# Optimization experiments

Measured on AMD Instinct MI355X. Metric: run time of the kernel, lower is better.

The kernel has to match this reference:

```python
import jax, jax.numpy as jnp
import numpy as np

B_SZ, L_SEQ, D_MODEL, D_STATE = 4, 2048, 1024, 16


def setup_inputs() -> dict:
    key = jax.random.key(0)
    ks = jax.random.split(key, 6)
    x = jax.random.normal(ks[0], (B_SZ, L_SEQ, D_MODEL), jnp.float32)
    # HiPPO-inspired init: A_log = log(arange(1..n)).clamp(min=-7), broadcast over channels
    A_log = jnp.clip(jnp.log(jnp.arange(1, D_STATE + 1, dtype=jnp.float32)), -7.0, None)
    A_log = jnp.broadcast_to(A_log[None, :], (D_MODEL, D_STATE)).astype(jnp.float32)
    B_param = 0.02 * jax.random.normal(ks[1], (D_MODEL, D_STATE), jnp.float32)
    C_param = 0.02 * jax.random.normal(ks[2], (D_MODEL, D_STATE), jnp.float32)
    log_dt = 0.01 * jax.random.normal(ks[3], (D_MODEL,), jnp.float32) - 4.0
    in_w = jax.random.normal(ks[4], (2 * D_MODEL, D_MODEL), jnp.float32) / np.sqrt(D_MODEL).astype(np.float32)
    in_b = jnp.zeros((2 * D_MODEL,), jnp.float32)
    out_w = jax.random.normal(ks[5], (D_MODEL, D_MODEL), jnp.float32) / np.sqrt(D_MODEL).astype(np.float32)
    out_b = jnp.zeros((D_MODEL,), jnp.float32)
    ln_g = jnp.ones((D_MODEL,), jnp.float32)
    ln_b = jnp.zeros((D_MODEL,), jnp.float32)
    return {"x": x, "A_log": A_log, "B_param": B_param, "C_param": C_param,
            "log_dt": log_dt, "in_w": in_w, "in_b": in_b, "out_w": out_w,
            "out_b": out_b, "ln_g": ln_g, "ln_b": ln_b}


def _ssm_scan(u, A_log, B_param, C_param, log_dt):
    # u: (B, L, D). Builds kernel h[t,d] = sum_n A_bar[d,n]^t * C[d,n]*B[d,n]*dt[d]
    # and applies a causal depthwise convolution (via FFT; same math as conv1d).
    L = u.shape[1]
    dt = jnp.clip(jnp.exp(log_dt), 1e-4, 1.0)                      # (D,)
    A_bar = jnp.exp(-jnp.exp(A_log) * dt[:, None])                 # ZOH discretisation (D,N)
    A_bar = jnp.clip(A_bar, 1e-8, 1.0 - 1e-8)
    log_A = jnp.log(A_bar)                                         # (D,N)
    t_idx = jnp.arange(L, dtype=jnp.float32)                       # (L,)
    A_powers = jnp.exp(t_idx[:, None, None] * log_A[None, :, :])   # (L,D,N)
    cb_dt = C_param * B_param * dt[:, None]                        # (D,N)
    kernel = jnp.einsum('ldn,dn->ld', A_powers, cb_dt)             # (L,D)
    # causal conv: y[b,t,d] = sum_{tau<=t} kernel[tau,d] * u[b,t-tau,d]
    n_fft = 2 * L
    Kf = jnp.fft.rfft(kernel, n=n_fft, axis=0)                     # (n_fft/2+1, D)
    Uf = jnp.fft.rfft(u, n=n_fft, axis=1)                          # (B, n_fft/2+1, D)
    y = jnp.fft.irfft(Uf * Kf[None], n=n_fft, axis=1)[:, :L]       # (B,L,D)
    return y.astype(u.dtype)


def reference(x, A_log, B_param, C_param, log_dt, in_w, in_b, out_w, out_b, ln_g, ln_b):
    x = x.astype(jnp.float32)
    residual = x
    # LayerNorm (eps=1e-5)
    mu = jnp.mean(x, axis=-1, keepdims=True)
    var = jnp.mean(jnp.square(x - mu), axis=-1, keepdims=True)
    xn = (x - mu) * jax.lax.rsqrt(var + 1e-5) * ln_g + ln_b
    xz = xn @ in_w.T + in_b                                        # (B,L,2D)
    x_proj, z = xz[..., :D_MODEL], xz[..., D_MODEL:]
    z = jax.nn.silu(z)
    y = _ssm_scan(x_proj, A_log, B_param, C_param, log_dt)
    y = y * z
    y = y @ out_w.T + out_b
    # dropout is identity in eval mode
    return jnp.clip(y + residual, -10.0, 10.0)
```

## Files before the change

### kernel.cpp

```cpp
#include <hip/hip_runtime.h>
#include <hip/hip_bf16.h>

#define D_MODEL 1024
#define D_STATE 16
#define L_SEQ 2048
#define B_SZ 4
#define M_ROWS (B_SZ * L_SEQ)
#define N_CHUNK 32
#define C_LEN 64

typedef __attribute__((ext_vector_type(8))) short short8;
typedef __attribute__((ext_vector_type(4))) float f32x4;

#define SBAR()  asm volatile("s_barrier" ::: "memory")
#define GATE(N) asm volatile("s_waitcnt vmcnt(" #N ") lgkmcnt(0)\n\ts_barrier" ::: "memory")

typedef const unsigned short __attribute__((address_space(1))) gas_us;
typedef unsigned short __attribute__((address_space(3))) las_us;
static __device__ __forceinline__ void gload16(const unsigned short* g, unsigned short* l) {
    __builtin_amdgcn_global_load_lds((gas_us*)g, (las_us*)l, 16, 0, 0);
}

static __device__ __forceinline__ unsigned short f2bf(float f) {
    unsigned int u = __float_as_uint(f);
    unsigned int r = (u + 0x7FFFu + ((u >> 16) & 1u)) >> 16;
    return (unsigned short)r;
}
static __device__ __forceinline__ float bf2f(unsigned short u) {
    return __uint_as_float(((unsigned int)u) << 16);
}

__global__ __launch_bounds__(256) void prep_kernel(const float* __restrict__ x,
                                                   const float* __restrict__ g,
                                                   const float* __restrict__ b,
                                                   unsigned short* __restrict__ xn,
                                                   const float* __restrict__ in_w,
                                                   unsigned short* __restrict__ w1,
                                                   const float* __restrict__ out_w,
                                                   unsigned short* __restrict__ w2) {
    __shared__ float sbuf[8];
    int bid = blockIdx.x;
    int t = threadIdx.x;
    if (bid < M_ROWS) {
        int row = bid;
        const float4* xr = (const float4*)(x + (size_t)row * D_MODEL);
        float4 v = xr[t];
        float s  = v.x + v.y + v.z + v.w;
        float ss = v.x * v.x + v.y * v.y + v.z * v.z + v.w * v.w;
        #pragma unroll
        for (int o = 32; o > 0; o >>= 1) {
            s  += __shfl_down(s,  o);
            ss += __shfl_down(ss, o);
        }
        int wid = t >> 6;
        if ((t & 63) == 0) { sbuf[wid] = s; sbuf[4 + wid] = ss; }
        __syncthreads();
        float S  = sbuf[0] + sbuf[1] + sbuf[2] + sbuf[3];
        float SS = sbuf[4] + sbuf[5] + sbuf[6] + sbuf[7];
        float mu  = S * (1.0f / D_MODEL);
        float var = SS * (1.0f / D_MODEL) - mu * mu;
        float inv = rsqrtf(var + 1e-5f);
        float4 gv = ((const float4*)g)[t];
        float4 bv = ((const float4*)b)[t];
        ushort4 o;
        o.x = f2bf((v.x - mu) * inv * gv.x + bv.x);
        o.y = f2bf((v.y - mu) * inv * gv.y + bv.y);
        o.z = f2bf((v.z - mu) * inv * gv.z + bv.z);
        o.w = f2bf((v.w - mu) * inv * gv.w + bv.w);
        ((ushort4*)(xn + (size_t)row * D_MODEL))[t] = o;
    } else if (bid < M_ROWS + 2048) {
        int i = (bid - M_ROWS) * 256 + t;
        float4 v = ((const float4*)in_w)[i];
        ushort4 o;
        o.x = f2bf(v.x); o.y = f2bf(v.y); o.z = f2bf(v.z); o.w = f2bf(v.w);
        ((ushort4*)w1)[i] = o;
    } else {
        int i = (bid - M_ROWS - 2048) * 256 + t;
        float4 v = ((const float4*)out_w)[i];
        ushort4 o;
        o.x = f2bf(v.x); o.y = f2bf(v.y); o.z = f2bf(v.z); o.w = f2bf(v.w);
        ((ushort4*)w2)[i] = o;
    }
}

#define STG(B_, MAT_, KH_, GPTR_, KOFF_) do { \
    unsigned short* d_ = lbase + (B_)*32768 + (MAT_)*16384 + (KH_)*8192 + wave*1024; \
    gload16((GPTR_) + (KOFF_), d_); \
    gload16((GPTR_) + 16*K + (KOFF_), d_ + 512); } while(0)

#define PH(B_, KS_, MG_, READB_, STAGE_, TAIL_) { \
    if (READB_) { \
        _Pragma("unroll") for (int j_ = 0; j_ < 4; ++j_) \
            bv[j_] = *(const short8*)(ldsB + (B_)*65536 + (KS_)*16384 + (wn*4 + j_)*1024); \
    } \
    short8 av[4]; \
    _Pragma("unroll") for (int i_ = 0; i_ < 4; ++i_) \
        av[i_] = *(const short8*)(ldsA + (B_)*65536 + (KS_)*16384 + (wm*8 + (MG_)*4 + i_)*1024); \
    STAGE_; \
    SBAR(); \
    asm volatile("s_waitcnt lgkmcnt(0)" ::: "memory"); \
    __builtin_amdgcn_s_setprio(1); \
    _Pragma("unroll") for (int i_ = 0; i_ < 4; ++i_) { \
        _Pragma("unroll") for (int j_ = 0; j_ < 4; ++j_) \
            acc[(MG_)*4 + i_][j_] = __builtin_amdgcn_mfma_f32_16x16x32_bf16( \
                av[i_], bv[j_], acc[(MG_)*4 + i_][j_], 0, 0, 0); } \
    __builtin_amdgcn_s_setprio(0); \
    TAIL_; \
}

__global__ __launch_bounds__(512, 1) void gemm1_kernel(const unsigned short* __restrict__ A,
                                                       const unsigned short* __restrict__ Bt,
                                                       const float* __restrict__ bias,
                                                       unsigned short* __restrict__ u_bf,
                                                       unsigned short* __restrict__ zs) {
    __shared__ __align__(16) unsigned short lds[2][32768];
    const int K = D_MODEL;

    int t = threadIdx.x;
    int lane = t & 63;
    int wave = t >> 6;
    int wm = wave >> 2;
    int wn = wave & 3;

    int bid = blockIdx.x;
    int swz = (bid & 7) * 32 + (bid >> 3);
    int m0 = (swz >> 3) * 256;
    int n0 = (swz & 7) * 256;

    int srow = lane >> 2;
    int sk = ((lane & 3) * 8) ^ ((lane & 32) >> 1);
    const unsigned short* gA = A  + (size_t)(m0 + wave * 32 + srow) * K + sk;
    const unsigned short* gB = Bt + (size_t)(n0 + wave * 32 + srow) * K + sk;

    unsigned short* lbase = &lds[0][0];

    int off_base = (lane & 15) * 64 + (((lane >> 4) * 16) ^ ((lane & 8) * 4));
    const char* ldsA = (const char*)lbase + off_base;
    const char* ldsB = (const char*)lbase + 32768 + off_base;

    f32x4 acc[8][4] = {};
    short8 bv[4];

    STG(0, 0, 0, gA, 0);  STG(0, 1, 0, gB, 0);
    STG(0, 0, 1, gA, 32); STG(0, 1, 1, gB, 32);
    STG(1, 0, 0, gA, 64); STG(1, 1, 0, gB, 64);
    GATE(4);

    int ko = 0;
    #pragma unroll 1
    for (int it = 0; it < 7; ++it) {
        PH(0, 0, 0, true,  STG(1, 0, 1, gA, ko + 96),  SBAR());
        PH(0, 0, 1, false, STG(1, 1, 1, gB, ko + 96),  SBAR());
        PH(0, 1, 0, true,  STG(0, 0, 0, gA, ko + 128), SBAR());
        PH(0, 1, 1, false, STG(0, 1, 0, gB, ko + 128), GATE(4));
        PH(1, 0, 0, true,  STG(0, 0, 1, gA, ko + 160), SBAR());
        PH(1, 0, 1, false, STG(0, 1, 1, gB, ko + 160), SBAR());
        PH(1, 1, 0, true,  STG(1, 0, 0, gA, ko + 192), SBAR());
        PH(1, 1, 1, false, STG(1, 1, 0, gB, ko + 192), GATE(4));
        ko += 128;
    }
    PH(0, 0, 0, true,  STG(1, 0, 1, gA, ko + 96), SBAR());
    PH(0, 0, 1, false, STG(1, 1, 1, gB, ko + 96), SBAR());
    PH(0, 1, 0, true,  (void)0, SBAR());
    PH(0, 1, 1, false, (void)0, GATE(0));
    PH(1, 0, 0, true,  (void)0, SBAR());
    PH(1, 0, 1, false, (void)0, SBAR());
    PH(1, 1, 0, true,  (void)0, SBAR());
    PH(1, 1, 1, false, (void)0, (void)0);

    int col = lane & 15;
    int quad = lane >> 4;
    float bs[4];
    #pragma unroll
    for (int jf = 0; jf < 4; ++jf) bs[jf] = bias[n0 + wn * 64 + jf * 16 + col];
    bool isU = (n0 < D_MODEL);
    int nbase = isU ? (n0 + wn * 64 + col) : (n0 - D_MODEL + wn * 64 + col);
    unsigned short* obase = isU ? u_bf : zs;
    #pragma unroll
    for (int i = 0; i < 8; ++i) {
        #pragma unroll
        for (int r = 0; r < 4; ++r) {
            int m = m0 + wm * 128 + i * 16 + quad * 4 + r;
            unsigned short* orow = obase + (size_t)m * D_MODEL + nbase;
            #pragma unroll
            for (int jf = 0; jf < 4; ++jf) {
                float v = acc[i][jf][r] + bs[jf];
                if (!isU) v = v / (1.0f + __expf(-v));
                orow[jf * 16] = f2bf(v);
            }
        }
    }
}

#define MFMA16(ACC, AV, BV) { \
    _Pragma("unroll") for (int i_ = 0; i_ < 4; ++i_) { \
        _Pragma("unroll") for (int jf_ = 0; jf_ < 4; ++jf_) \
            ACC[i_][jf_] = __builtin_amdgcn_mfma_f32_16x16x32_bf16( \
                AV[i_], BV[jf_], ACC[i_][jf_], 0, 0, 0); } }

#define STAGE2(J) { size_t ko_ = (size_t)(J) * 32; int so_ = ((J) & 3) * 12288; \
    gload16(pA0 + ko_, dA + so_); gload16(pB0 + ko_, dB0 + so_); gload16(pB1 + ko_, dB1 + so_); }

#define G2_TILE(J, DOSTAGE, TRAIL) { \
    const int slot_ = (J) & 3; \
    const char* rA_ = ldsA_rd + slot_ * 24576; \
    const char* rB_ = ldsB_rd + slot_ * 24576; \
    short8 av[4], bv[4]; \
    _Pragma("unroll") for (int i_ = 0; i_ < 4; ++i_) av[i_] = *(const short8*)(rA_ + i_ * 1024); \
    _Pragma("unroll") for (int j_ = 0; j_ < 4; ++j_) bv[j_] = *(const short8*)(rB_ + j_ * 1024); \
    if (DOSTAGE) { STAGE2((J) + 3); } \
    SBAR(); \
    __builtin_amdgcn_s_setprio(1); \
    MFMA16(acc, av, bv); \
    __builtin_amdgcn_s_setprio(0); \
    TRAIL; \
}

__global__ __launch_bounds__(512, 2) void gemm2_kernel(const unsigned short* __restrict__ A,
                                                       const unsigned short* __restrict__ Bt,
                                                       const float* __restrict__ bias,
                                                       float* __restrict__ out_f,
                                                       const float* __restrict__ resid) {
    __shared__ __align__(16) unsigned short lds[4][12288];
    const int K = D_MODEL;

    int t = threadIdx.x;
    int lane = t & 63;
    int wave = t >> 6;
    int wm = wave >> 2;
    int wn = wave & 3;

    int bid = blockIdx.x;
    int swz = (bid & 7) * 32 + (bid >> 3);
    int m0 = (swz >> 2) * 128;
    int n0 = (swz & 3) * 256;

    int srow = lane >> 2;
    int sk = ((lane & 3) * 8) ^ ((lane & 32) >> 1);
    const unsigned short* pA0 = A  + (size_t)(m0 + wave * 16 + srow) * K + sk;
    const unsigned short* pB0 = Bt + (size_t)(n0 + wave * 16 + srow) * K + sk;
    const unsigned short* pB1 = pB0 + (size_t)128 * K;

    unsigned short* dA  = &lds[0][wave * 512];
    unsigned short* dB0 = &lds[0][4096 + wave * 512];
    unsigned short* dB1 = &lds[0][8192 + wave * 512];

    int off_base = (lane & 15) * 64 + (((lane >> 4) * 16) ^ ((lane & 8) * 4));
    const char* ldsA_rd = (const char*)(&lds[0][0]) + wm * 4096 + off_base;
    const char* ldsB_rd = (const char*)(&lds[0][0]) + 8192 + wn * 4096 + off_base;

    f32x4 acc[4][4] = {};

    STAGE2(0); STAGE2(1); STAGE2(2);
    GATE(6);

    #pragma unroll 1
    for (int j = 0; j < 29; ++j) { G2_TILE(j, true, GATE(6)); }
    G2_TILE(29, false, GATE(3));
    G2_TILE(30, false, GATE(0));
    G2_TILE(31, false, (void)0);

    int col = lane & 15;
    int quad = lane >> 4;
    float bs[4];
    #pragma unroll
    for (int jf = 0; jf < 4; ++jf) bs[jf] = bias[n0 + wn * 64 + jf * 16 + col];
    #pragma unroll
    for (int i = 0; i < 4; ++i) {
        #pragma unroll
        for (int r = 0; r < 4; ++r) {
            int m = m0 + wm * 64 + i * 16 + quad * 4 + r;
            const float* rrow = resid + (size_t)m * D_MODEL + n0 + wn * 64 + col;
            float* orow = out_f + (size_t)m * D_MODEL + n0 + wn * 64 + col;
            #pragma unroll
            for (int jf = 0; jf < 4; ++jf) {
                float y = acc[i][jf][r] + bs[jf] + rrow[jf * 16];
                y = fminf(10.0f, fmaxf(-10.0f, y));
                orow[jf * 16] = y;
            }
        }
    }
}

__global__ __launch_bounds__(512) void scan_fused_kernel(const unsigned short* __restrict__ u,
                                                         const unsigned short* __restrict__ zs,
                                                         const float* __restrict__ A_log,
                                                         const float* __restrict__ Bp,
                                                         const float* __restrict__ Cp,
                                                         const float* __restrict__ log_dt,
                                                         unsigned short* __restrict__ yz) {
    __shared__ float S[N_CHUNK][D_STATE][17];

    int bid = blockIdx.x;
    int l  = (bid & 7) * 32 + (bid >> 3);
    int b  = l >> 6;
    int dg = l & 63;
    int t  = threadIdx.x;
    int c  = t >> 4;
    int dl = t & 15;
    int d  = dg * 16 + dl;

    float dt = fminf(1.0f, fmaxf(1e-4f, __expf(log_dt[d])));
    float ab[D_STATE];
    #pragma unroll
    for (int n = 0; n < D_STATE; n++) {
        float a = __expf(-__expf(A_log[d * D_STATE + n]) * dt);
        ab[n] = fminf(1.0f - 1e-8f, fmaxf(1e-8f, a));
    }

    size_t row0 = (size_t)(b * L_SEQ + c * C_LEN);
    const unsigned short* up = u + row0 * D_MODEL + d;

    unsigned int uc[32];
    float P[D_STATE];
    #pragma unroll
    for (int n = 0; n < D_STATE; n++) P[n] = 0.0f;
    #pragma unroll
    for (int tt = 0; tt < 32; tt++) {
        unsigned int lo = up[(size_t)(2 * tt) * D_MODEL];
        unsigned int hi = up[(size_t)(2 * tt + 1) * D_MODEL];
        uc[tt] = lo | (hi << 16);
        float u0 = __uint_as_float(lo << 16);
        float u1 = __uint_as_float(hi << 16);
        #pragma unroll
        for (int n = 0; n < D_STATE; n++) P[n] = fmaf(ab[n], P[n], u0);
        #pragma unroll
        for (int n = 0; n < D_STATE; n++) P[n] = fmaf(ab[n], P[n], u1);
    }

    #pragma unroll
    for (int n = 0; n < D_STATE; n++) S[c][n][dl] = P[n];

    float m[D_STATE];
    #pragma unroll
    for (int n = 0; n < D_STATE; n++) {
        float a2 = ab[n];
        #pragma unroll
        for (int q = 0; q < 6; q++) a2 = a2 * a2;
        m[n] = a2;
    }
    __syncthreads();

    #pragma unroll
    for (int k = 1; k < N_CHUNK; k <<= 1) {
        float tmp[D_STATE];
        #pragma unroll
        for (int n = 0; n < D_STATE; n++) tmp[n] = (c >= k) ? S[c - k][n][dl] : 0.0f;
        __syncthreads();
        #pragma unroll
        for (int n = 0; n < D_STATE; n++) {
            P[n] = fmaf(m[n], tmp[n], P[n]);
            S[c][n][dl] = P[n];
        }
        #pragma unroll
        for (int n = 0; n < D_STATE; n++) m[n] = m[n] * m[n];
        __syncthreads();
    }

    float s2[D_STATE];
    #pragma unroll
    for (int n = 0; n < D_STATE; n++) s2[n] = (c == 0) ? 0.0f : S[c - 1][n][dl];

    float cb[D_STATE];
    #pragma unroll
    for (int n = 0; n < D_STATE; n++)
        cb[n] = Cp[d * D_STATE + n] * Bp[d * D_STATE + n] * dt;

    const unsigned short* zp = zs + row0 * D_MODEL + d;
    unsigned short* yp = yz + row0 * D_MODEL + d;

    #pragma unroll
    for (int tt = 0; tt < 32; tt++) {
        unsigned int w = uc[tt];
        float u0 = __uint_as_float(w << 16);
        float u1 = __uint_as_float(w & 0xFFFF0000u);
        float y0 = 0.0f, y1 = 0.0f;
        #pragma unroll
        for (int n = 0; n < D_STATE; n++) s2[n] = fmaf(ab[n], s2[n], u0);
        #pragma unroll
        for (int n = 0; n < D_STATE; n++) y0 = fmaf(cb[n], s2[n], y0);
        #pragma unroll
        for (int n = 0; n < D_STATE; n++) s2[n] = fmaf(ab[n], s2[n], u1);
        #pragma unroll
        for (int n = 0; n < D_STATE; n++) y1 = fmaf(cb[n], s2[n], y1);
        float z0 = bf2f(zp[(size_t)(2 * tt) * D_MODEL]);
        float z1 = bf2f(zp[(size_t)(2 * tt + 1) * D_MODEL]);
        yp[(size_t)(2 * tt) * D_MODEL]     = f2bf(y0 * z0);
        yp[(size_t)(2 * tt + 1) * D_MODEL] = f2bf(y1 * z1);
    }
}

extern "C" void kernel_launch(void* const* d_in, const int* in_sizes, int n_in,
                              void* d_out, int out_size, void* d_ws, size_t ws_size,
                              hipStream_t stream) {
    const float* x       = (const float*)d_in[0];
    const float* A_log   = (const float*)d_in[1];
    const float* B_param = (const float*)d_in[2];
    const float* C_param = (const float*)d_in[3];
    const float* log_dt  = (const float*)d_in[4];
    const float* in_w    = (const float*)d_in[5];
    const float* in_b    = (const float*)d_in[6];
    const float* out_w   = (const float*)d_in[7];
    const float* out_b   = (const float*)d_in[8];
    const float* ln_g    = (const float*)d_in[9];
    const float* ln_b    = (const float*)d_in[10];
    float* out = (float*)d_out;

    char* ws = (char*)d_ws;
    size_t off = 0;
    unsigned short* xn = (unsigned short*)(ws + off); off += (size_t)M_ROWS * D_MODEL * 2;
    unsigned short* w1 = (unsigned short*)(ws + off); off += (size_t)2 * D_MODEL * D_MODEL * 2;
    unsigned short* u  = (unsigned short*)(ws + off); off += (size_t)M_ROWS * D_MODEL * 2;
    unsigned short* zs = (unsigned short*)(ws + off); off += (size_t)M_ROWS * D_MODEL * 2;
    unsigned short* yz = (unsigned short*)(ws + off); off += (size_t)M_ROWS * D_MODEL * 2;
    unsigned short* w2 = (unsigned short*)(ws + off); off += (size_t)D_MODEL * D_MODEL * 2;

    prep_kernel<<<M_ROWS + 2048 + 1024, 256, 0, stream>>>(x, ln_g, ln_b, xn, in_w, w1, out_w, w2);

    gemm1_kernel<<<256, 512, 0, stream>>>(xn, w1, in_b, u, zs);

    scan_fused_kernel<<<256, 512, 0, stream>>>(u, zs, A_log, B_param, C_param, log_dt, yz);

    gemm2_kernel<<<256, 512, 0, stream>>>(yz, w2, out_b, out, x);
}
```

Before: 197.2 us.

## Stage scan input slab in LDS and vectorize z-gating global traffic

The scan kernel now bulk-loads the block's whole 2048x16 bf16 input slab into shared memory with global_load_lds 16-byte transfers, replacing per-thread 2-byte strided global reads. The register cache of u values is dropped, the scan re-reads u from LDS, and y is written back in place into the slab. The z multiply and output store become a separate coalesced short8 pass over global memory. This targets uncoalesced 2-byte accesses with a large row stride, at the cost of 64KB of LDS per block (lower occupancy), an extra barrier, and bf16 rounding of y before the gating multiply.

```diff
diff --git a/kernel.cpp b/kernel.cpp
--- a/kernel.cpp
+++ b/kernel.cpp
@@ -289,6 +289,7 @@
                                                          const float* __restrict__ Cp,
                                                          const float* __restrict__ log_dt,
                                                          unsigned short* __restrict__ yz) {
+    __shared__ __align__(16) unsigned short uslab[L_SEQ * 16];
     __shared__ float S[N_CHUNK][D_STATE][17];
 
     int bid = blockIdx.x;
@@ -299,6 +300,16 @@
     int c  = t >> 4;
     int dl = t & 15;
     int d  = dg * 16 + dl;
+    int lane = t & 63;
+    int wave = t >> 6;
+
+    {
+        const unsigned short* src = u + ((size_t)b * L_SEQ + wave * 32 + (lane >> 1)) * D_MODEL
+                                      + dg * 16 + (lane & 1) * 8;
+        #pragma unroll
+        for (int i = 0; i < 8; ++i)
+            gload16(src + (size_t)i * 256 * D_MODEL, uslab + (i * 256 + wave * 32) * 16);
+    }
 
     float dt = fminf(1.0f, fmaxf(1e-4f, __expf(log_dt[d])));
     float ab[D_STATE];
@@ -307,25 +318,23 @@
         float a = __expf(-__expf(A_log[d * D_STATE + n]) * dt);
         ab[n] = fminf(1.0f - 1e-8f, fmaxf(1e-8f, a));
     }
-
-    size_t row0 = (size_t)(b * L_SEQ + c * C_LEN);
-    const unsigned short* up = u + row0 * D_MODEL + d;
-
-    unsigned int uc[32];
+    float cb[D_STATE];
+    #pragma unroll
+    for (int n = 0; n < D_STATE; n++)
+        cb[n] = Cp[d * D_STATE + n] * Bp[d * D_STATE + n] * dt;
+
+    asm volatile("s_waitcnt vmcnt(0)" ::: "memory");
+    __syncthreads();
+
+    const unsigned short* rcol = uslab + (c * 64) * 16 + dl;
     float P[D_STATE];
     #pragma unroll
     for (int n = 0; n < D_STATE; n++) P[n] = 0.0f;
-    #pragma unroll
-    for (int tt = 0; tt < 32; tt++) {
-        unsigned int lo = up[(size_t)(2 * tt) * D_MODEL];
-        unsigned int hi = up[(size_t)(2 * tt + 1) * D_MODEL];
-        uc[tt] = lo | (hi << 16);
-        float u0 = __uint_as_float(lo << 16);
-        float u1 = __uint_as_float(hi << 16);
-        #pragma unroll
-        for (int n = 0; n < D_STATE; n++) P[n] = fmaf(ab[n], P[n], u0);
-        #pragma unroll
-        for (int n = 0; n < D_STATE; n++) P[n] = fmaf(ab[n], P[n], u1);
+    #pragma unroll 4
+    for (int tt = 0; tt < C_LEN; tt++) {
+        float uv = bf2f(rcol[tt * 16]);
+        #pragma unroll
+        for (int n = 0; n < D_STATE; n++) P[n] = fmaf(ab[n], P[n], uv);
     }
 
     #pragma unroll
@@ -361,32 +370,34 @@
     #pragma unroll
     for (int n = 0; n < D_STATE; n++) s2[n] = (c == 0) ? 0.0f : S[c - 1][n][dl];
 
-    float cb[D_STATE];
-    #pragma unroll
-    for (int n = 0; n < D_STATE; n++)
-        cb[n] = Cp[d * D_STATE + n] * Bp[d * D_STATE + n] * dt;
-
-    const unsigned short* zp = zs + row0 * D_MODEL + d;
-    unsigned short* yp = yz + row0 * D_MODEL + d;
-
-    #pragma unroll
-    for (int tt = 0; tt < 32; tt++) {
-        unsigned int w = uc[tt];
-        float u0 = __uint_as_float(w << 16);
-        float u1 = __uint_as_float(w & 0xFFFF0000u);
-        float y0 = 0.0f, y1 = 0.0f;
-        #pragma unroll
-        for (int n = 0; n < D_STATE; n++) s2[n] = fmaf(ab[n], s2[n], u0);
-        #pragma unroll
-        for (int n = 0; n < D_STATE; n++) y0 = fmaf(cb[n], s2[n], y0);
-        #pragma unroll
-        for (int n = 0; n < D_STATE; n++) s2[n] = fmaf(ab[n], s2[n], u1);
-        #pragma unroll
-        for (int n = 0; n < D_STATE; n++) y1 = fmaf(cb[n], s2[n], y1);
-        float z0 = bf2f(zp[(size_t)(2 * tt) * D_MODEL]);
-        float z1 = bf2f(zp[(size_t)(2 * tt + 1) * D_MODEL]);
-        yp[(size_t)(2 * tt) * D_MODEL]     = f2bf(y0 * z0);
-        yp[(size_t)(2 * tt + 1) * D_MODEL] = f2bf(y1 * z1);
+    unsigned short* wcol = uslab + (c * 64) * 16 + dl;
+    #pragma unroll 4
+    for (int tt = 0; tt < C_LEN; tt++) {
+        float uv = bf2f(wcol[tt * 16]);
+        #pragma unroll
+        for (int n = 0; n < D_STATE; n++) s2[n] = fmaf(ab[n], s2[n], uv);
+        float y = 0.0f;
+        #pragma unroll
+        for (int n = 0; n < D_STATE; n++) y = fmaf(cb[n], s2[n], y);
+        wcol[tt * 16] = f2bf(y);
+    }
+    __syncthreads();
+
+    {
+        size_t gbase = (size_t)b * L_SEQ * D_MODEL + (size_t)dg * 16;
+        #pragma unroll
+        for (int i = 0; i < 8; ++i) {
+            int idx = i * 512 + t;
+            int row = idx >> 1, half = idx & 1;
+            size_t go = gbase + (size_t)row * D_MODEL + half * 8;
+            short8 zv = *(const short8*)(zs + go);
+            short8 yv = *(const short8*)(uslab + idx * 8);
+            short8 o;
+            #pragma unroll
+            for (int e = 0; e < 8; ++e)
+                o[e] = (short)f2bf(bf2f((unsigned short)yv[e]) * bf2f((unsigned short)zv[e]));
+            *(short8*)(yz + go) = o;
+        }
     }
 }
 
```

After: 199.3 us. Within noise of the previous version (+1.1%).

## Retile output GEMM to 256x128 blocks with 2-stage double-buffered 64-wide K pipeline

Applied to the files above, without the earlier changes.

Changes the second GEMM from 128x256 tiles with a 4-slot 32-wide K ring to 256x128 tiles arranged as a 4x2 wave grid. The K loop now runs in 64-wide steps, split into two half-phases over two LDS buffers, and loads are interleaved with MFMA phases. Launch bounds drop to one block per CU because LDS use grows to 96KB. The aim is better operand reuse per LDS load and fewer barriers per K element, at the cost of lower occupancy and a more complex prefetch schedule.

```diff
diff --git a/kernel.cpp b/kernel.cpp
--- a/kernel.cpp
+++ b/kernel.cpp
@@ -192,73 +192,81 @@
     }
 }
 
-#define MFMA16(ACC, AV, BV) { \
+#define STGA2(B_, KH_, TK_) do { \
+    unsigned short* d_ = lbase2 + (B_)*24576 + (KH_)*8192 + wave*1024; \
+    gload16(gA2 + (size_t)(TK_)*64 + (KH_)*32, d_); \
+    gload16(gA2 + (size_t)16*K + (size_t)(TK_)*64 + (KH_)*32, d_ + 512); } while(0)
+#define STGB2(B_, KH_, TK_) do { \
+    unsigned short* d_ = lbase2 + (B_)*24576 + 16384 + (KH_)*4096 + wave*512; \
+    gload16(gB2 + (size_t)(TK_)*64 + (KH_)*32, d_); } while(0)
+
+#define PH2(B_, KH_, STAGE_, TAIL_) { \
+    short8 av[4], bv[4]; \
+    _Pragma("unroll") for (int j_ = 0; j_ < 4; ++j_) \
+        bv[j_] = *(const short8*)(ldsB2 + (B_)*49152 + (KH_)*8192 + (wn*4 + j_)*1024); \
+    _Pragma("unroll") for (int i_ = 0; i_ < 4; ++i_) \
+        av[i_] = *(const short8*)(ldsA2 + (B_)*49152 + (KH_)*16384 + (wm*4 + i_)*1024); \
+    STAGE_; \
+    SBAR(); \
+    asm volatile("s_waitcnt lgkmcnt(0)" ::: "memory"); \
+    __builtin_amdgcn_s_setprio(1); \
     _Pragma("unroll") for (int i_ = 0; i_ < 4; ++i_) { \
-        _Pragma("unroll") for (int jf_ = 0; jf_ < 4; ++jf_) \
-            ACC[i_][jf_] = __builtin_amdgcn_mfma_f32_16x16x32_bf16( \
-                AV[i_], BV[jf_], ACC[i_][jf_], 0, 0, 0); } }
-
-#define STAGE2(J) { size_t ko_ = (size_t)(J) * 32; int so_ = ((J) & 3) * 12288; \
-    gload16(pA0 + ko_, dA + so_); gload16(pB0 + ko_, dB0 + so_); gload16(pB1 + ko_, dB1 + so_); }
-
-#define G2_TILE(J, DOSTAGE, TRAIL) { \
-    const int slot_ = (J) & 3; \
-    const char* rA_ = ldsA_rd + slot_ * 24576; \
-    const char* rB_ = ldsB_rd + slot_ * 24576; \
-    short8 av[4], bv[4]; \
-    _Pragma("unroll") for (int i_ = 0; i_ < 4; ++i_) av[i_] = *(const short8*)(rA_ + i_ * 1024); \
-    _Pragma("unroll") for (int j_ = 0; j_ < 4; ++j_) bv[j_] = *(const short8*)(rB_ + j_ * 1024); \
-    if (DOSTAGE) { STAGE2((J) + 3); } \
-    SBAR(); \
-    __builtin_amdgcn_s_setprio(1); \
-    MFMA16(acc, av, bv); \
+        _Pragma("unroll") for (int j_ = 0; j_ < 4; ++j_) \
+            acc[i_][j_] = __builtin_amdgcn_mfma_f32_16x16x32_bf16( \
+                av[i_], bv[j_], acc[i_][j_], 0, 0, 0); } \
     __builtin_amdgcn_s_setprio(0); \
-    TRAIL; \
-}
-
-__global__ __launch_bounds__(512, 2) void gemm2_kernel(const unsigned short* __restrict__ A,
+    TAIL_; \
+}
+
+__global__ __launch_bounds__(512, 1) void gemm2_kernel(const unsigned short* __restrict__ A,
                                                        const unsigned short* __restrict__ Bt,
                                                        const float* __restrict__ bias,
                                                        float* __restrict__ out_f,
                                                        const float* __restrict__ resid) {
-    __shared__ __align__(16) unsigned short lds[4][12288];
+    __shared__ __align__(16) unsigned short lds[2][24576];
     const int K = D_MODEL;
 
     int t = threadIdx.x;
     int lane = t & 63;
     int wave = t >> 6;
-    int wm = wave >> 2;
-    int wn = wave & 3;
+    int wm = wave >> 1;
+    int wn = wave & 1;
 
     int bid = blockIdx.x;
     int swz = (bid & 7) * 32 + (bid >> 3);
-    int m0 = (swz >> 2) * 128;
-    int n0 = (swz & 3) * 256;
+    int m0 = (swz >> 3) * 256;
+    int n0 = (swz & 7) * 128;
 
     int srow = lane >> 2;
     int sk = ((lane & 3) * 8) ^ ((lane & 32) >> 1);
-    const unsigned short* pA0 = A  + (size_t)(m0 + wave * 16 + srow) * K + sk;
-    const unsigned short* pB0 = Bt + (size_t)(n0 + wave * 16 + srow) * K + sk;
-    const unsigned short* pB1 = pB0 + (size_t)128 * K;
-
-    unsigned short* dA  = &lds[0][wave * 512];
-    unsigned short* dB0 = &lds[0][4096 + wave * 512];
-    unsigned short* dB1 = &lds[0][8192 + wave * 512];
+    const unsigned short* gA2 = A  + (size_t)(m0 + wave * 32 + srow) * K + sk;
+    const unsigned short* gB2 = Bt + (size_t)(n0 + wave * 16 + srow) * K + sk;
+
+    unsigned short* lbase2 = &lds[0][0];
 
     int off_base = (lane & 15) * 64 + (((lane >> 4) * 16) ^ ((lane & 8) * 4));
-    const char* ldsA_rd = (const char*)(&lds[0][0]) + wm * 4096 + off_base;
-    const char* ldsB_rd = (const char*)(&lds[0][0]) + 8192 + wn * 4096 + off_base;
+    const char* ldsA2 = (const char*)lbase2 + off_base;
+    const char* ldsB2 = (const char*)lbase2 + 32768 + off_base;
 
     f32x4 acc[4][4] = {};
 
-    STAGE2(0); STAGE2(1); STAGE2(2);
-    GATE(6);
-
+    STGA2(0, 0, 0); STGA2(0, 1, 0); STGB2(0, 0, 0); STGB2(0, 1, 0);
+    STGA2(1, 0, 1); STGB2(1, 0, 1);
+    GATE(3);
+
+    int tk = 0;
     #pragma unroll 1
-    for (int j = 0; j < 29; ++j) { G2_TILE(j, true, GATE(6)); }
-    G2_TILE(29, false, GATE(3));
-    G2_TILE(30, false, GATE(0));
-    G2_TILE(31, false, (void)0);
+    for (int it = 0; it < 7; ++it) {
+        PH2(0, 0, { STGA2(1, 1, tk + 1); STGB2(1, 1, tk + 1); }, SBAR());
+        PH2(0, 1, { STGA2(0, 0, tk + 2); STGB2(0, 0, tk + 2); }, GATE(3));
+        PH2(1, 0, { STGA2(0, 1, tk + 2); STGB2(0, 1, tk + 2); }, SBAR());
+        PH2(1, 1, { STGA2(1, 0, tk + 3); STGB2(1, 0, tk + 3); }, GATE(3));
+        tk += 2;
+    }
+    PH2(0, 0, { STGA2(1, 1, 15); STGB2(1, 1, 15); }, SBAR());
+    PH2(0, 1, (void)0, GATE(0));
+    PH2(1, 0, (void)0, SBAR());
+    PH2(1, 1, (void)0, (void)0);
 
     int col = lane & 15;
     int quad = lane >> 4;
```

Result: no change. 198.8 us (+0.8%).
